# Kernel optimization log

Measured on AMD Instinct MI355X. Metric: run time of the kernel, lower is better.

## Reference

```python
import jax, jax.numpy as jnp
import numpy as np

EPS = 1e-8  # RMSNormMultiHead default eps (forward passes self.eps)


def rms_norm_multihead(x, weight):
    # x: (B, L, H, d); normalize over last dim in float32, then scale per (H, d)
    x32 = x.astype(jnp.float32)
    normed = x32 * jax.lax.rsqrt(jnp.mean(x32 * x32, axis=-1, keepdims=True) + EPS)
    return normed.astype(x.dtype) * weight


def setup_inputs() -> dict:
    key = jax.random.key(0)
    k0, k1, k2 = jax.random.split(key, 3)
    B, L, D, H = 2, 1024, 1024, 16
    d = D // H
    X = jax.random.normal(k0, (B, L, D), dtype=jnp.float32)
    Wq = jax.random.normal(k1, (D, D), dtype=jnp.float32) * 0.02  # q_proj weight (out, in)
    Wv = jax.random.normal(k2, (D, D), dtype=jnp.float32) * 0.02  # v_proj weight (out, in)
    q_norm_w = jnp.ones((H, d), dtype=jnp.float32)
    v_norm_w = jnp.ones((H, d), dtype=jnp.float32)
    return {"X": X, "Wq": Wq, "Wv": Wv, "q_norm_w": q_norm_w, "v_norm_w": v_norm_w}


def reference(X, Wq, Wv, q_norm_w, v_norm_w):
    B, L, D = X.shape
    H, d = q_norm_w.shape
    K = X.reshape(B, L, H, d)
    Q = rms_norm_multihead((X @ Wq.T).reshape(B, L, H, d), q_norm_w)
    V = rms_norm_multihead((X @ Wv.T).reshape(B, L, H, d), v_norm_w)
    # cumulative outer-product KV state: (B, L, H, d, e)
    W = jnp.cumsum(jnp.einsum('blhd,blhe->blhde', K, V), axis=1)
    out = jnp.einsum('blhd,blhde->blhe', Q, W).reshape(B, L, D)
    return out
```

## Files before the change

kernel.cpp:

```cpp
#include <hip/hip_runtime.h>

#define BB 2
#define LL 1024
#define DD 1024
#define HH 16
#define NC 16
#define EPSF 1e-8f

typedef __attribute__((ext_vector_type(8))) short bf16x8;
typedef __attribute__((ext_vector_type(4))) float f32x4;
typedef unsigned short u16;

static __device__ inline u16 f2bf(float f) {
    unsigned int u = __builtin_bit_cast(unsigned int, f);
    u += 0x7fff + ((u >> 16) & 1);
    return (u16)(u >> 16);
}
static __device__ inline float bf2f(u16 v) {
    unsigned int u = ((unsigned int)v) << 16;
    return __builtin_bit_cast(float, u);
}
static __device__ inline void gload_lds16(const u16* g, u16* l) {
    __builtin_amdgcn_global_load_lds((const __attribute__((address_space(1))) void*)g,
                                     (__attribute__((address_space(3))) void*)l, 16, 0, 0);
}

__global__ __launch_bounds__(256) void cvt_k(const float* __restrict__ X,
                                             const float* __restrict__ Wq,
                                             const float* __restrict__ Wv,
                                             u16* __restrict__ Xb,
                                             u16* __restrict__ Wqb,
                                             u16* __restrict__ Wvb)
{
    int i = (blockIdx.x * 256 + threadIdx.x) * 4;
    const float* s; u16* d; int off;
    if (i < 2*1024*1024)      { s = X;  d = Xb;  off = i; }
    else if (i < 3*1024*1024) { s = Wq; d = Wqb; off = i - 2*1024*1024; }
    else                      { s = Wv; d = Wvb; off = i - 3*1024*1024; }
    float4 v = *(const float4*)(s + off);
    ushort4 o;
    o.x = f2bf(v.x); o.y = f2bf(v.y); o.z = f2bf(v.z); o.w = f2bf(v.w);
    *(ushort4*)(d + off) = o;
}

__global__ __launch_bounds__(256) void gemm_fused(const u16* __restrict__ Xb,
                                                  const u16* __restrict__ Wqb,
                                                  const u16* __restrict__ Wvb,
                                                  const float* __restrict__ qw,
                                                  const float* __restrict__ vw,
                                                  u16* __restrict__ Qb,
                                                  u16* __restrict__ Vb)
{
    const int K = DD, N = DD;
    const u16* W = blockIdx.z ? Wvb : Wqb;
    const float* nw = blockIdx.z ? vw : qw;
    u16* Y = blockIdx.z ? Vb : Qb;
    __shared__ u16 As0[128 * 32], As1[128 * 32];
    __shared__ u16 Bs0[64 * 32],  Bs1[64 * 32];

    const int tid = threadIdx.x, w = tid >> 6, lane = tid & 63;
    const int quad = lane >> 4, l16 = lane & 15;
    const int m0 = blockIdx.y * 128, n0 = blockIdx.x * 64;
    const int lrow = lane >> 2, lcol = (lane & 3) * 8;

    const u16* gA0 = Xb + (size_t)(m0 + w*16 + lrow) * K + lcol;
    const u16* gA1 = gA0 + (size_t)64 * K;
    const u16* gB0 = W + (size_t)(n0 + w*16 + lrow) * K + lcol;
    u16* lA0_0 = &As0[(w*16) * 32];      u16* lA0_1 = &As1[(w*16) * 32];
    u16* lA1_0 = &As0[(64 + w*16) * 32]; u16* lA1_1 = &As1[(64 + w*16) * 32];
    u16* lB0_0 = &Bs0[(w*16) * 32];      u16* lB0_1 = &Bs1[(w*16) * 32];

    f32x4 acc[2][4] = {};
    for (int k0 = 0; k0 < K; k0 += 64) {
        gload_lds16(gA0 + k0,      lA0_0);
        gload_lds16(gA0 + k0 + 32, lA0_1);
        gload_lds16(gA1 + k0,      lA1_0);
        gload_lds16(gA1 + k0 + 32, lA1_1);
        gload_lds16(gB0 + k0,      lB0_0);
        gload_lds16(gB0 + k0 + 32, lB0_1);
        __syncthreads();
        #pragma unroll
        for (int hh = 0; hh < 2; ++hh) {
            const u16* Ah = hh ? As1 : As0;
            const u16* Bh = hh ? Bs1 : Bs0;
            bf16x8 af[2], bfr[4];
            #pragma unroll
            for (int i = 0; i < 2; ++i)
                af[i] = *(const bf16x8*)&Ah[(w*32 + i*16 + l16) * 32 + quad*8];
            #pragma unroll
            for (int j = 0; j < 4; ++j)
                bfr[j] = *(const bf16x8*)&Bh[(j*16 + l16) * 32 + quad*8];
            #pragma unroll
            for (int i = 0; i < 2; ++i)
                #pragma unroll
                for (int j = 0; j < 4; ++j)
                    acc[i][j] = __builtin_amdgcn_mfma_f32_16x16x32_bf16(af[i], bfr[j], acc[i][j], 0, 0, 0);
        }
        __syncthreads();
    }

    float wv4[4];
    #pragma unroll
    for (int j = 0; j < 4; ++j) wv4[j] = nw[n0 + j*16 + l16];
    #pragma unroll
    for (int i = 0; i < 2; ++i) {
        float ss[4];
        #pragma unroll
        for (int r = 0; r < 4; ++r) {
            float s = 0.f;
            #pragma unroll
            for (int j = 0; j < 4; ++j) s += acc[i][j][r] * acc[i][j][r];
            ss[r] = s;
        }
        #pragma unroll
        for (int off = 1; off < 16; off <<= 1)
            #pragma unroll
            for (int r = 0; r < 4; ++r) ss[r] += __shfl_xor(ss[r], off, 64);
        float sc[4];
        #pragma unroll
        for (int r = 0; r < 4; ++r) sc[r] = rsqrtf(ss[r] * (1.f/64.f) + EPSF);
        #pragma unroll
        for (int r = 0; r < 4; ++r) {
            u16* yp = Y + (size_t)(m0 + w*32 + i*16 + quad*4 + r) * N + n0;
            #pragma unroll
            for (int j = 0; j < 4; ++j)
                yp[j*16 + l16] = f2bf(acc[i][j][r] * sc[r] * wv4[j]);
        }
    }
}

__global__ __launch_bounds__(256) void kv_chunk(const u16* __restrict__ Xb,
                                                const u16* __restrict__ Vb,
                                                u16* __restrict__ S)
{
    const int c = blockIdx.x & 15, bh = blockIdx.x >> 4;
    const int h = bh & 15, b = bh >> 4;
    __shared__ u16 Kt[64][72];
    __shared__ u16 Vt[64][72];
    const int tid = threadIdx.x;
    {
        const int row = tid >> 2, q = tid & 3;
        size_t gbase = (size_t)(b*LL + c*64 + row) * DD + h*64 + q*16;
        u16 kk[16], vv[16];
        #pragma unroll
        for (int i = 0; i < 16; i += 4) {
            *(ushort4*)&kk[i] = *(const ushort4*)(Xb + gbase + i);
            *(ushort4*)&vv[i] = *(const ushort4*)(Vb + gbase + i);
        }
        #pragma unroll
        for (int i = 0; i < 16; ++i) {
            Kt[q*16 + i][row] = kk[i];
            Vt[q*16 + i][row] = vv[i];
        }
    }
    __syncthreads();
    const int w = tid >> 6, lane = tid & 63, quad = lane >> 4, l16 = lane & 15;
    const int me = (w & 1) * 32, nd = (w >> 1) * 32;
    f32x4 acc[2][2] = {};
    #pragma unroll
    for (int k0 = 0; k0 < 64; k0 += 32) {
        bf16x8 av[2], bv[2];
        #pragma unroll
        for (int i = 0; i < 2; ++i)
            av[i] = *(const bf16x8*)&Vt[me + i*16 + l16][k0 + quad*8];
        #pragma unroll
        for (int j = 0; j < 2; ++j)
            bv[j] = *(const bf16x8*)&Kt[nd + j*16 + l16][k0 + quad*8];
        #pragma unroll
        for (int i = 0; i < 2; ++i)
            #pragma unroll
            for (int j = 0; j < 2; ++j)
                acc[i][j] = __builtin_amdgcn_mfma_f32_16x16x32_bf16(av[i], bv[j], acc[i][j], 0, 0, 0);
    }
    u16* Sp = S + ((size_t)blockIdx.x << 12) + w*1024;
    #pragma unroll
    for (int i = 0; i < 2; ++i)
        #pragma unroll
        for (int j = 0; j < 2; ++j)
            #pragma unroll
            for (int r = 0; r < 4; ++r)
                Sp[(i*2 + j)*256 + r*64 + lane] = f2bf(acc[i][j][r]);
}

__global__ __launch_bounds__(256) void out_k2(const u16* __restrict__ Xb,
                                              const u16* __restrict__ Qb,
                                              const u16* __restrict__ Vb,
                                              const u16* __restrict__ S,
                                              float* __restrict__ out)
{
    const int c = 15 - (blockIdx.x & 15);
    const int bh = blockIdx.x >> 4;
    const int h = bh & 15, b = bh >> 4;
    __shared__ u16 Qs[64][72];
    __shared__ u16 Ks[64][72];
    __shared__ u16 Vt[64][72];
    __shared__ u16 St[64][72];
    const int tid = threadIdx.x;
    {
        const int row = tid >> 2, q = tid & 3;
        size_t gbase = (size_t)(b*LL + c*64 + row) * DD + h*64 + q*16;
        u16 vv[16];
        #pragma unroll
        for (int i = 0; i < 16; i += 4) {
            *(ushort4*)&Qs[row][q*16 + i] = *(const ushort4*)(Qb + gbase + i);
            *(ushort4*)&Ks[row][q*16 + i] = *(const ushort4*)(Xb + gbase + i);
            *(ushort4*)&vv[i] = *(const ushort4*)(Vb + gbase + i);
        }
        #pragma unroll
        for (int i = 0; i < 16; ++i)
            Vt[q*16 + i][row] = vv[i];
        float facc[16] = {};
        const u16* Sbase = S + ((size_t)(bh * NC) << 12);
        for (int cp = 0; cp < c; ++cp) {
            const u16* Sc = Sbase + ((size_t)cp << 12);
            #pragma unroll
            for (int jj = 0; jj < 4; ++jj) {
                ushort4 sv = *(const ushort4*)(Sc + tid*4 + jj*1024);
                facc[jj*4+0] += bf2f(sv.x);
                facc[jj*4+1] += bf2f(sv.y);
                facc[jj*4+2] += bf2f(sv.z);
                facc[jj*4+3] += bf2f(sv.w);
            }
        }
        #pragma unroll
        for (int jj = 0; jj < 4; ++jj) {
            int g = tid * 4;
            int ij = (g >> 8) & 3, r = (g >> 6) & 3, ln = g & 63;
            int e = (jj & 1)*32 + (ij >> 1)*16 + (ln >> 4)*4 + r;
            int d = (jj >> 1)*32 + (ij & 1)*16 + (ln & 15);
            ushort4 o;
            o.x = f2bf(facc[jj*4+0]);
            o.y = f2bf(facc[jj*4+1]);
            o.z = f2bf(facc[jj*4+2]);
            o.w = f2bf(facc[jj*4+3]);
            *(ushort4*)&St[e][d] = o;
        }
    }
    __syncthreads();
    const int w = tid >> 6, lane = tid & 63, quad = lane >> 4, l16 = lane & 15;
    const int mo = (w & 1) * 32, no = (w >> 1) * 32;

    f32x4 pacc[2][2] = {};
    #pragma unroll
    for (int k0 = 0; k0 < 64; k0 += 32) {
        bf16x8 aq[2], bk[2];
        #pragma unroll
        for (int i = 0; i < 2; ++i)
            aq[i] = *(const bf16x8*)&Qs[mo + i*16 + l16][k0 + quad*8];
        #pragma unroll
        for (int j = 0; j < 2; ++j)
            bk[j] = *(const bf16x8*)&Ks[no + j*16 + l16][k0 + quad*8];
        #pragma unroll
        for (int i = 0; i < 2; ++i)
            #pragma unroll
            for (int j = 0; j < 2; ++j)
                pacc[i][j] = __builtin_amdgcn_mfma_f32_16x16x32_bf16(aq[i], bk[j], pacc[i][j], 0, 0, 0);
    }
    __syncthreads();
    #pragma unroll
    for (int i = 0; i < 2; ++i)
        #pragma unroll
        for (int j = 0; j < 2; ++j)
            #pragma unroll
            for (int r = 0; r < 4; ++r) {
                int l  = mo + i*16 + quad*4 + r;
                int lp = no + j*16 + l16;
                Ks[l][lp] = (lp <= l) ? f2bf(pacc[i][j][r]) : (u16)0;
            }
    __syncthreads();

    f32x4 acc[2][2] = {};
    #pragma unroll
    for (int k0 = 0; k0 < 64; k0 += 32) {
        bf16x8 a1[2], b1[2], a2[2], b2[2];
        #pragma unroll
        for (int i = 0; i < 2; ++i) {
            a1[i] = *(const bf16x8*)&Ks[mo + i*16 + l16][k0 + quad*8];
            a2[i] = *(const bf16x8*)&Qs[mo + i*16 + l16][k0 + quad*8];
        }
        #pragma unroll
        for (int j = 0; j < 2; ++j) {
            b1[j] = *(const bf16x8*)&Vt[no + j*16 + l16][k0 + quad*8];
            b2[j] = *(const bf16x8*)&St[no + j*16 + l16][k0 + quad*8];
        }
        #pragma unroll
        for (int i = 0; i < 2; ++i)
            #pragma unroll
            for (int j = 0; j < 2; ++j) {
                acc[i][j] = __builtin_amdgcn_mfma_f32_16x16x32_bf16(a1[i], b1[j], acc[i][j], 0, 0, 0);
                acc[i][j] = __builtin_amdgcn_mfma_f32_16x16x32_bf16(a2[i], b2[j], acc[i][j], 0, 0, 0);
            }
    }
    float* op = out + (size_t)(b*LL + c*64) * DD + h*64;
    #pragma unroll
    for (int i = 0; i < 2; ++i)
        #pragma unroll
        for (int j = 0; j < 2; ++j)
            #pragma unroll
            for (int r = 0; r < 4; ++r)
                op[(size_t)(mo + i*16 + quad*4 + r) * DD + no + j*16 + l16] = acc[i][j][r];
}

extern "C" void kernel_launch(void* const* d_in, const int* in_sizes, int n_in,
                              void* d_out, int out_size, void* d_ws, size_t ws_size,
                              hipStream_t stream) {
    const float* X  = (const float*)d_in[0];
    const float* Wq = (const float*)d_in[1];
    const float* Wv = (const float*)d_in[2];
    const float* qw = (const float*)d_in[3];
    const float* vw = (const float*)d_in[4];
    float* out = (float*)d_out;

    u16* Xb  = (u16*)d_ws;
    u16* Wqb = Xb  + (size_t)2*1024*1024;
    u16* Wvb = Wqb + (size_t)1024*1024;
    u16* Qb  = Wvb + (size_t)1024*1024;
    u16* Vb  = Qb  + (size_t)2*1024*1024;
    u16* S   = Vb  + (size_t)2*1024*1024;

    cvt_k<<<4096, 256, 0, stream>>>(X, Wq, Wv, Xb, Wqb, Wvb);
    gemm_fused<<<dim3(16, 16, 2), 256, 0, stream>>>(Xb, Wqb, Wvb, qw, vw, Qb, Vb);
    kv_chunk<<<BB*HH*NC, 256, 0, stream>>>(Xb, Vb, S);
    out_k2<<<BB*HH*NC, 256, 0, stream>>>(Xb, Qb, Vb, S, out);
}
```

Baseline: 101.9 us.

## Fuse per-chunk KV outer-product state into the V projection GEMM epilogue

Removes the separate kv_chunk kernel. The V-projection blocks now write their normalized V tile transposed into a shared arena, load the matching X (K) tiles, and compute the two 64x64 chunk states with MFMA before storing S. This saves one kernel launch and the round trip of re-reading V from global memory. In exchange, the GEMM kernel's shared-memory footprint and epilogue grow, and the z=1 blocks carry extra tail work that the z=0 blocks do not.

```diff
diff --git a/kernel.cpp b/kernel.cpp
--- a/kernel.cpp
+++ b/kernel.cpp
@@ -49,14 +49,23 @@
                                                   const float* __restrict__ qw,
                                                   const float* __restrict__ vw,
                                                   u16* __restrict__ Qb,
-                                                  u16* __restrict__ Vb)
+                                                  u16* __restrict__ Vb,
+                                                  u16* __restrict__ S)
 {
     const int K = DD, N = DD;
     const u16* W = blockIdx.z ? Wvb : Wqb;
     const float* nw = blockIdx.z ? vw : qw;
     u16* Y = blockIdx.z ? Vb : Qb;
-    __shared__ u16 As0[128 * 32], As1[128 * 32];
-    __shared__ u16 Bs0[64 * 32],  Bs1[64 * 32];
+    __shared__ u16 arena[18432];
+    u16* As0 = arena;
+    u16* As1 = arena + 4096;
+    u16* Bs0 = arena + 8192;
+    u16* Bs1 = arena + 10240;
+    typedef u16 (*tile_t)[72];
+    tile_t Kt0 = (tile_t)(arena);
+    tile_t Kt1 = (tile_t)(arena + 4608);
+    tile_t Vt0 = (tile_t)(arena + 9216);
+    tile_t Vt1 = (tile_t)(arena + 13824);
 
     const int tid = threadIdx.x, w = tid >> 6, lane = tid & 63;
     const int quad = lane >> 4, l16 = lane & 15;
@@ -121,65 +130,70 @@
         for (int r = 0; r < 4; ++r) sc[r] = rsqrtf(ss[r] * (1.f/64.f) + EPSF);
         #pragma unroll
         for (int r = 0; r < 4; ++r) {
-            u16* yp = Y + (size_t)(m0 + w*32 + i*16 + quad*4 + r) * N + n0;
-            #pragma unroll
-            for (int j = 0; j < 4; ++j)
-                yp[j*16 + l16] = f2bf(acc[i][j][r] * sc[r] * wv4[j]);
-        }
-    }
-}
-
-__global__ __launch_bounds__(256) void kv_chunk(const u16* __restrict__ Xb,
-                                                const u16* __restrict__ Vb,
-                                                u16* __restrict__ S)
-{
-    const int c = blockIdx.x & 15, bh = blockIdx.x >> 4;
-    const int h = bh & 15, b = bh >> 4;
-    __shared__ u16 Kt[64][72];
-    __shared__ u16 Vt[64][72];
-    const int tid = threadIdx.x;
+            const int lr = w*32 + i*16 + quad*4 + r;
+            u16* yp = Y + (size_t)(m0 + lr) * N + n0;
+            tile_t Vt = (lr & 64) ? Vt1 : Vt0;
+            #pragma unroll
+            for (int j = 0; j < 4; ++j) {
+                u16 o = f2bf(acc[i][j][r] * sc[r] * wv4[j]);
+                yp[j*16 + l16] = o;
+                if (blockIdx.z) Vt[j*16 + l16][lr & 63] = o;
+            }
+        }
+    }
+
+    if (blockIdx.z == 0) return;
+
     {
         const int row = tid >> 2, q = tid & 3;
-        size_t gbase = (size_t)(b*LL + c*64 + row) * DD + h*64 + q*16;
-        u16 kk[16], vv[16];
-        #pragma unroll
-        for (int i = 0; i < 16; i += 4) {
-            *(ushort4*)&kk[i] = *(const ushort4*)(Xb + gbase + i);
-            *(ushort4*)&vv[i] = *(const ushort4*)(Vb + gbase + i);
-        }
-        #pragma unroll
-        for (int i = 0; i < 16; ++i) {
-            Kt[q*16 + i][row] = kk[i];
-            Vt[q*16 + i][row] = vv[i];
+        #pragma unroll
+        for (int p = 0; p < 2; ++p) {
+            const u16* gk = Xb + (size_t)(m0 + p*64 + row) * DD + n0 + q*16;
+            u16 kk[16];
+            #pragma unroll
+            for (int i = 0; i < 16; i += 4)
+                *(ushort4*)&kk[i] = *(const ushort4*)(gk + i);
+            tile_t Kt = p ? Kt1 : Kt0;
+            #pragma unroll
+            for (int i = 0; i < 16; ++i)
+                Kt[q*16 + i][row] = kk[i];
         }
     }
     __syncthreads();
-    const int w = tid >> 6, lane = tid & 63, quad = lane >> 4, l16 = lane & 15;
+
+    const int b = m0 >> 10, h = blockIdx.x;
+    const int c0 = (m0 & 1023) >> 6;
+    const int bh = b*16 + h;
     const int me = (w & 1) * 32, nd = (w >> 1) * 32;
-    f32x4 acc[2][2] = {};
-    #pragma unroll
-    for (int k0 = 0; k0 < 64; k0 += 32) {
-        bf16x8 av[2], bv[2];
+    #pragma unroll
+    for (int cc = 0; cc < 2; ++cc) {
+        tile_t Kt = cc ? Kt1 : Kt0;
+        tile_t Vt = cc ? Vt1 : Vt0;
+        f32x4 sacc[2][2] = {};
+        #pragma unroll
+        for (int k0 = 0; k0 < 64; k0 += 32) {
+            bf16x8 av[2], bv[2];
+            #pragma unroll
+            for (int i = 0; i < 2; ++i)
+                av[i] = *(const bf16x8*)&Vt[me + i*16 + l16][k0 + quad*8];
+            #pragma unroll
+            for (int j = 0; j < 2; ++j)
+                bv[j] = *(const bf16x8*)&Kt[nd + j*16 + l16][k0 + quad*8];
+            #pragma unroll
+            for (int i = 0; i < 2; ++i)
+                #pragma unroll
+                for (int j = 0; j < 2; ++j)
+                    sacc[i][j] = __builtin_amdgcn_mfma_f32_16x16x32_bf16(av[i], bv[j], sacc[i][j], 0, 0, 0);
+        }
+        u16* Sp = S + ((size_t)(bh*NC + c0 + cc) << 12) + w*1024;
         #pragma unroll
         for (int i = 0; i < 2; ++i)
-            av[i] = *(const bf16x8*)&Vt[me + i*16 + l16][k0 + quad*8];
-        #pragma unroll
-        for (int j = 0; j < 2; ++j)
-            bv[j] = *(const bf16x8*)&Kt[nd + j*16 + l16][k0 + quad*8];
-        #pragma unroll
-        for (int i = 0; i < 2; ++i)
             #pragma unroll
             for (int j = 0; j < 2; ++j)
-                acc[i][j] = __builtin_amdgcn_mfma_f32_16x16x32_bf16(av[i], bv[j], acc[i][j], 0, 0, 0);
-    }
-    u16* Sp = S + ((size_t)blockIdx.x << 12) + w*1024;
-    #pragma unroll
-    for (int i = 0; i < 2; ++i)
-        #pragma unroll
-        for (int j = 0; j < 2; ++j)
-            #pragma unroll
-            for (int r = 0; r < 4; ++r)
-                Sp[(i*2 + j)*256 + r*64 + lane] = f2bf(acc[i][j][r]);
+                #pragma unroll
+                for (int r = 0; r < 4; ++r)
+                    Sp[(i*2 + j)*256 + r*64 + lane] = f2bf(sacc[i][j][r]);
+    }
 }
 
 __global__ __launch_bounds__(256) void out_k2(const u16* __restrict__ Xb,
@@ -319,7 +333,6 @@
     u16* S   = Vb  + (size_t)2*1024*1024;
 
     cvt_k<<<4096, 256, 0, stream>>>(X, Wq, Wv, Xb, Wqb, Wvb);
-    gemm_fused<<<dim3(16, 16, 2), 256, 0, stream>>>(Xb, Wqb, Wvb, qw, vw, Qb, Vb);
-    kv_chunk<<<BB*HH*NC, 256, 0, stream>>>(Xb, Vb, S);
+    gemm_fused<<<dim3(16, 16, 2), 256, 0, stream>>>(Xb, Wqb, Wvb, qw, vw, Qb, Vb, S);
     out_k2<<<BB*HH*NC, 256, 0, stream>>>(Xb, Qb, Vb, S, out);
 }
```

After: 102.1 us. Within noise of the previous version (+0.2%).
